# Kernel optimization log

Measured on AMD Instinct MI355X. Metric: run time of the kernel, lower is better.

The kernel has to match this reference:

```python
import jax, jax.numpy as jnp
import numpy as np

H = 128   # hidden_size
NL = 3    # num_layers
R = 32    # water_rows (Water2sea_slice_num)
O = 48    # water_cols (Original_slice_len)
B = 64    # batch_size
F = 32    # input_size
L = R + O - 1  # Water2sea_slice_len (wavefront length)


def setup_inputs():
    key = jax.random.key(0)
    k1, k2, k3, k4 = jax.random.split(key, 4)
    stdv = 1.0 / np.sqrt(H)
    inp = jax.random.normal(k1, (B, R, O, F), dtype=jnp.float32)
    W_first = jax.random.uniform(k2, (6 * H, F + 2 * H), minval=-stdv, maxval=stdv, dtype=jnp.float32)
    W_other = jax.random.uniform(k3, (NL - 1, 6 * H, 4 * H), minval=-stdv, maxval=stdv, dtype=jnp.float32)
    Bias = jax.random.uniform(k4, (NL, 6 * H), minval=-stdv, maxval=stdv, dtype=jnp.float32)
    return {"input": inp, "W_first": W_first, "W_other": W_other, "Bias": Bias,
            "batch_size": B, "input_size": F, "flag": 0}


def _forward(inp, W_first, W_other, Bias, batch_size, input_size, flag):
    # permute: flag==0 -> [rows, batch, cols, feat]
    x = jnp.transpose(inp, (2, 0, 1, 3)) if flag == 1 else jnp.transpose(inp, (1, 0, 2, 3))
    Rn, bs, On, Fn = x.shape
    Ln = Rn + On - 1
    # wavefront-shifted input: row r occupies slices [r, r+On) (input_transfer)
    padded = jnp.pad(x, ((0, 0), (0, 0), (0, Rn - 1), (0, 0)))                 # [R,B,L,F]
    shifted = jax.vmap(lambda t, r: jnp.roll(t, r, axis=1))(padded, jnp.arange(Rn))
    a0 = shifted.reshape(Rn * bs, Ln, Fn)
    # bias applied to row-group g at slice s iff (s < Rn) and (g <= s)  [faithful to linear()]
    s_idx = jnp.arange(Ln)[:, None]
    g_idx = jnp.arange(Rn)[None, :]
    bias_mask = ((g_idx <= s_idx) & (s_idx < Rn)).astype(jnp.float32)          # [L,R]
    bias_mask = jnp.repeat(bias_mask, bs, axis=1)[..., None]                   # [L,RB,1]

    def run_layer(a, W, bvec):
        # a: [RB, L, feat]; W: [6H, feat+2H]; bvec: [6H]
        def step(carry, xs):
            h_row, h_col = carry
            a_s, m_s = xs
            z = jnp.concatenate([h_row, h_col, a_s], axis=-1)
            gate = z @ W.T + m_s * bvec                                        # [RB,6H]
            sig = jax.nn.sigmoid(gate[:, :4 * H])
            tnh = jnp.tanh(gate[:, 4 * H:])
            ur, orow, uc, ocol = jnp.split(sig, 4, axis=-1)
            ir, ic = jnp.split(tnh, 2, axis=-1)
            h_row_n = jnp.tanh((1.0 - ur) * h_row + ur * ir) * orow
            h_col_n = jnp.tanh((1.0 - uc) * h_col + uc * ic) * ocol
            out = jnp.concatenate([h_row_n, h_col_n], axis=-1)
            h_col_roll = jnp.roll(h_col_n, bs, axis=0)  # transfer col hidden to next row
            return (h_row_n, h_col_roll), (out, h_row_n, h_col_n)
        h0 = jnp.zeros((Rn * bs, H), a.dtype)
        _, (outs, hrows, hcols) = jax.lax.scan(step, (h0, h0), (jnp.swapaxes(a, 0, 1), bias_mask))
        return outs, hrows, hcols  # each [L, RB, *]

    row_saves, col_saves = [], []
    a = a0
    for layer in range(NL):
        W = W_first if layer == 0 else W_other[layer - 1]
        outs, hrows, hcols = run_layer(a, W, Bias[layer])
        hrows = hrows.reshape(Ln, Rn, bs, H)
        hcols = hcols.reshape(Ln, Rn, bs, H)
        # row r finishes at slice On-1+r; col hidden of last row-group saved for slices >= Rn-1
        row_saves.append(hrows[On - 1 + jnp.arange(Rn), jnp.arange(Rn)])       # [R,B,H]
        col_saves.append(hcols[Rn - 1:, Rn - 1])                               # [O,B,H]
        a = jnp.swapaxes(outs, 0, 1)                                           # [RB,L,2H]; dropout p=0 -> identity
    output_all_slice = a
    hidden_row_all = jnp.transpose(jnp.stack(row_saves), (2, 0, 1, 3))         # [B,NL,R,H]
    hidden_col_all = jnp.transpose(jnp.stack(col_saves), (2, 0, 1, 3))         # [B,NL,O,H]
    return output_all_slice, hidden_row_all, hidden_col_all


def reference(input, W_first, W_other, Bias, batch_size, input_size, flag):
    return _forward(input, W_first, W_other, Bias, batch_size, input_size, flag)
```

## Files before the change

kernel.cpp:

```cpp
#include <hip/hip_runtime.h>
#include <stdint.h>

#define HH   128
#define NLAY 3
#define RR   32
#define OO   48
#define BBX  64
#define FFX  32
#define LLX  (RR + OO - 1)
#define RBr  (RR * BBX)
#define N6   (6 * HH)
#define TSTEPS (LLX + NLAY - 1)
#define NBLOCKS 192

typedef unsigned short u16;
typedef __attribute__((ext_vector_type(8))) short short8;
typedef __attribute__((ext_vector_type(4))) float f32x4;

#define OFF_ABUF0 ((size_t)0)
#define SZ_ABUF0  ((size_t)LLX * RBr * FFX * 2)
#define OFF_HZ    (OFF_ABUF0 + SZ_ABUF0)
#define SZ_HZ     ((size_t)NLAY * 2 * RBr * 256 * 2)
#define OFF_BAR   (OFF_HZ + SZ_HZ)
#define SZ_BAR    ((size_t)4096)
#define SZ_STATE  (SZ_HZ + SZ_BAR)

__device__ __forceinline__ u16 f2b(float x) {
  uint32_t u = __float_as_uint(x);
  return (u16)((u + 0x7FFFu + ((u >> 16) & 1u)) >> 16);
}
__device__ __forceinline__ float rcp_(float x) { return __builtin_amdgcn_rcpf(x); }
__device__ __forceinline__ float sigmoidf_(float x) {
  return rcp_(1.0f + __expf(-x));
}
__device__ __forceinline__ float tanhf_(float x) {
  return 1.0f - 2.0f * rcp_(__expf(2.0f * x) + 1.0f);
}

__global__ __launch_bounds__(256) void k_prep_input(const float* __restrict__ inp,
                                                    u16* __restrict__ abuf0) {
  int idx = blockIdx.x * 256 + threadIdx.x;
  if (idx >= LLX * RBr * FFX) return;
  int f   = idx & (FFX - 1);
  int row = (idx >> 5) & (RBr - 1);
  int s   = idx / (RBr * FFX);
  int g = row >> 6, b = row & 63;
  int o = s - g;
  float v = (o >= 0 && o < OO) ? inp[((b * RR + g) * OO + o) * FFX + f] : 0.0f;
  abuf0[idx] = f2b(v);
}

__global__ __launch_bounds__(256) void k_zero(uint32_t* __restrict__ p, size_t nwords) {
  size_t i = (size_t)blockIdx.x * 256 + threadIdx.x;
  size_t stride = (size_t)gridDim.x * 256;
  for (; i < nwords; i += stride) p[i] = 0u;
}

__device__ __forceinline__ void step_barrier(uint32_t* barC, uint32_t target, bool light) {
  __syncthreads();
  if (threadIdx.x == 0) {
    if (!light) __threadfence();
    __hip_atomic_fetch_add(barC, 1u, __ATOMIC_RELAXED, __HIP_MEMORY_SCOPE_AGENT);
    while (__hip_atomic_load(barC, __ATOMIC_RELAXED, __HIP_MEMORY_SCOPE_AGENT) < target)
      __builtin_amdgcn_s_sleep(1);
    if (!light) __threadfence();
  }
  __syncthreads();
  if (light) asm volatile("buffer_inv" ::: "memory");
}

template <int KK>
__device__ __forceinline__ void stage_w(const float* __restrict__ Wsrc, int jblk,
                                        u16* __restrict__ Wl) {
  constexpr int NFRAG = (KK / 32) * 6;
  for (int e = threadIdx.x; e < NFRAG * 64; e += 1024) {
    int kcm = e >> 6, ln = e & 63;
    int kc = kcm / 6, m = kcm - kc * 6;
    int fr2 = ln & 15, hi2 = ln >> 4;
    int srow = m * 128 + jblk * 16 + fr2;
    const float* src = Wsrc + (size_t)srow * KK + kc * 32 + hi2 * 8;
    short8 v;
#pragma unroll
    for (int x = 0; x < 8; ++x) v[x] = (short)f2b(src[x]);
    *(short8*)&Wl[(size_t)e * 8] = v;
  }
}

template <int KK>
__device__ __forceinline__ void persist_body(char* __restrict__ ws,
                                             const float* __restrict__ Bias_l,
                                             float* __restrict__ out,
                                             int layer, int jblk, int bblk, bool light,
                                             u16* __restrict__ Wl,
                                             float* __restrict__ hcl,
                                             uint32_t* __restrict__ barC) {
  constexpr int NCH = KK / 32;
  const int tid = threadIdx.x;
  const int lane = tid & 63, w = tid >> 6;
  const int fr = lane & 15, hi = lane >> 4;

  const int g0   = w * 2 + (fr >> 3);
  const int bcol = bblk * 8 + (fr & 7);
  const int arow = g0 * 64 + bcol;
  const int arp  = ((g0 + 1) & 31) * 64 + bcol;
  const int j = jblk * 16 + fr;
  const u16* wfrag = &Wl[lane * 8];
  float bia[6];
#pragma unroll
  for (int m = 0; m < 6; ++m) bia[m] = Bias_l[m * 128 + j];

  u16*   hz_base  = (u16*)(ws + OFF_HZ) + (size_t)layer * 2 * RBr * 256;
  u16*   hzp_base = (u16*)(ws + OFF_HZ) + (size_t)(layer - 1) * 2 * RBr * 256;
  u16*   abuf0    = (u16*)(ws + OFF_ABUF0);
  float* hid_row  = out + (size_t)RBr * LLX * 256;
  float* hid_col  = hid_row + (size_t)BBX * NLAY * RR * HH;

  float hr_reg[4];
#pragma unroll
  for (int q = 0; q < 4; ++q) hr_reg[q] = 0.0f;

  for (int t = 0; t < TSTEPS; ++t) {
    const int s = t - layer;
    if (s >= 0 && s < LLX) {
      const int sW = s & 1, sR = sW ^ 1;
      const u16* hzR = hz_base + (size_t)sR * RBr * 256;
      u16*       hzW = hz_base + (size_t)sW * RBr * 256;
      const u16* hzP = hzp_base + (size_t)sW * RBr * 256;
      const u16* ab_s = abuf0 + (size_t)s * RBr * FFX;
      const float* hcR = hcl + sR * 4352;
      float*       hcW = hcl + sW * 4352;

      if (w * 2 <= s) {
        auto LDK = [&](int kc) -> short8 {
          if (kc < 8)
            return *(const short8*)&hzR[arow * 256 + kc * 32 + hi * 8];
          if constexpr (KK == 288) {
            return *(const short8*)&ab_s[arow * FFX + hi * 8];
          } else {
            if (kc < 12)
              return *(const short8*)&hzP[arow * 256 + (kc - 8) * 32 + hi * 8];
            return *(const short8*)&hzP[arp * 256 + 128 + (kc - 12) * 32 + hi * 8];
          }
        };

        f32x4 z4 = {0.f, 0.f, 0.f, 0.f};
        f32x4 acc[6];
#pragma unroll
        for (int m = 0; m < 6; ++m) acc[m] = z4;

        short8 ring[3];
        ring[0] = LDK(0);
        ring[1] = LDK(1);
        ring[2] = LDK(2);
        __builtin_amdgcn_s_setprio(1);
#pragma unroll
        for (int kc = 0; kc < NCH; ++kc) {
          short8 a = ring[kc % 3];
          if (kc + 3 < NCH) ring[kc % 3] = LDK(kc + 3);
#pragma unroll
          for (int m = 0; m < 6; ++m) {
            short8 bv = *(const short8*)&wfrag[(size_t)(kc * 6 + m) * 512];
            acc[m] = __builtin_amdgcn_mfma_f32_16x16x32_bf16(a, bv, acc[m], 0, 0, 0);
          }
        }
        __builtin_amdgcn_s_setprio(0);

        const int g = w * 2 + (hi >> 1);
        const int gp = (g + 1) & (RR - 1);
        const float msk = (g <= s && s < RR) ? 1.0f : 0.0f;
        float mb[6];
#pragma unroll
        for (int m = 0; m < 6; ++m) mb[m] = msk * bia[m];
#pragma unroll
        for (int q = 0; q < 4; ++q) {
          const int lb = (hi & 1) * 4 + q;
          const int b  = bblk * 8 + lb;
          const int row = g * 64 + b;
          const int lrow = g * 8 + lb;
          const int rp = gp * 64 + b;
          const int lrp = gp * 8 + lb;
          float ur  = sigmoidf_(acc[0][q] + mb[0]);
          float orw = sigmoidf_(acc[1][q] + mb[1]);
          float uc  = sigmoidf_(acc[2][q] + mb[2]);
          float oc  = sigmoidf_(acc[3][q] + mb[3]);
          float ir  = tanhf_(acc[4][q] + mb[4]);
          float ic  = tanhf_(acc[5][q] + mb[5]);
          float hr_o = hr_reg[q];
          float hc_o = hcR[lrow * 17 + fr];
          float hr_n = tanhf_((1.0f - ur) * hr_o + ur * ir) * orw;
          float hc_n = tanhf_((1.0f - uc) * hc_o + uc * ic) * oc;
          hr_reg[q] = hr_n;
          hcW[lrp * 17 + fr] = hc_n;
          hzW[row * 256 + j] = f2b(hr_n);
          hzW[rp * 256 + HH + j] = f2b(hc_n);
          if (layer == 2) {
            out[((size_t)row * LLX + s) * 256 + j] = hr_n;
            out[((size_t)row * LLX + s) * 256 + HH + j] = hc_n;
          }
          if (s - g == OO - 1)
            hid_row[((size_t)(b * NLAY + layer) * RR + g) * HH + j] = hr_n;
          if (g == RR - 1 && s >= RR - 1)
            hid_col[((size_t)(b * NLAY + layer) * OO + (s - (RR - 1))) * HH + j] = hc_n;
        }
      } else {
        const int g = w * 2 + (hi >> 1);
        const int gp = (g + 1) & (RR - 1);
#pragma unroll
        for (int q = 0; q < 4; ++q) {
          const int lb = (hi & 1) * 4 + q;
          const int b  = bblk * 8 + lb;
          const int row = g * 64 + b;
          const int rp = gp * 64 + b;
          const int lrp = gp * 8 + lb;
          hcW[lrp * 17 + fr] = 0.0f;
          hzW[row * 256 + j] = 0;
          hzW[rp * 256 + HH + j] = 0;
          if (layer == 2) {
            out[((size_t)row * LLX + s) * 256 + j] = 0.0f;
            out[((size_t)row * LLX + s) * 256 + HH + j] = 0.0f;
          }
        }
      }
    }
    step_barrier(barC, 24u * (uint32_t)(t + 1), light);
  }
}

__global__ __launch_bounds__(1024, 4) void k_persist(char* __restrict__ ws,
                                                     const float* __restrict__ Wf,
                                                     const float* __restrict__ Wo,
                                                     const float* __restrict__ Bias,
                                                     float* __restrict__ out) {
  __shared__ u16 Wl[49152];
  __shared__ float hcl[8704];
  __shared__ uint32_t sh_light;
  const int bx = blockIdx.x;
  const int layer = bx >> 6, jblk = (bx >> 3) & 7, bblk = bx & 7;
  const int tid = threadIdx.x;

  if (layer == 0) stage_w<288>(Wf, jblk, Wl);
  else            stage_w<512>(Wo + (size_t)(layer - 1) * N6 * 512, jblk, Wl);
  for (int e = tid; e < 8704; e += 1024) hcl[e] = 0.0f;

  uint32_t xcc;
  asm volatile("s_getreg_b32 %0, hwreg(20, 0, 4)" : "=s"(xcc));
  uint32_t* barG  = (uint32_t*)(ws + OFF_BAR);
  uint32_t* barC  = (uint32_t*)(ws + OFF_BAR + 128 + (size_t)bblk * 128);
  uint32_t* table = (uint32_t*)(ws + OFF_BAR + 2048);
  __syncthreads();
  if (tid == 0) {
    __hip_atomic_store(&table[bx], xcc, __ATOMIC_RELAXED, __HIP_MEMORY_SCOPE_AGENT);
    __hip_atomic_fetch_add(barG, 1u, __ATOMIC_RELEASE, __HIP_MEMORY_SCOPE_AGENT);
    while (__hip_atomic_load(barG, __ATOMIC_ACQUIRE, __HIP_MEMORY_SCOPE_AGENT) < NBLOCKS)
      __builtin_amdgcn_s_sleep(1);
    uint32_t lt = 1u;
    for (int q2 = 0; q2 < 24; ++q2) {
      uint32_t v = __hip_atomic_load(&table[q2 * 8 + bblk], __ATOMIC_RELAXED,
                                     __HIP_MEMORY_SCOPE_AGENT);
      lt &= (v == xcc) ? 1u : 0u;
    }
    sh_light = lt;
  }
  __syncthreads();
  const bool light = (sh_light != 0u);

  const float* bias_l = Bias + layer * N6;
  if (layer == 0)
    persist_body<288>(ws, bias_l, out, 0, jblk, bblk, light, Wl, hcl, barC);
  else
    persist_body<512>(ws, bias_l, out, layer, jblk, bblk, light, Wl, hcl, barC);
}

extern "C" void kernel_launch(void* const* d_in, const int* in_sizes, int n_in,
                              void* d_out, int out_size, void* d_ws, size_t ws_size,
                              hipStream_t stream) {
  const float* inp  = (const float*)d_in[0];
  const float* Wf   = (const float*)d_in[1];
  const float* Wo   = (const float*)d_in[2];
  const float* Bias = (const float*)d_in[3];
  float* out = (float*)d_out;
  char* ws = (char*)d_ws;
  (void)in_sizes; (void)n_in; (void)out_size; (void)ws_size;

  k_prep_input<<<(LLX * RBr * FFX) / 256, 256, 0, stream>>>(inp, (u16*)(ws + OFF_ABUF0));
  k_zero<<<2048, 256, 0, stream>>>((uint32_t*)(ws + OFF_HZ), SZ_STATE / 4);
  k_persist<<<NBLOCKS, 1024, 0, stream>>>(ws, Wf, Wo, Bias, out);
}
```

Measured before the change: 770.8 us.

## Replace atomic-counter barrier with flag/epoch barrier and overlap output stores

Replaces the shared fetch-add step barrier with per-block arrival flags on separate cache lines, polled by a leader block that then publishes an epoch word all others spin on. The fp32 output and hidden-state stores move after the arrival signal, so they overlap the barrier wait instead of delaying it. The A-operand load ring is deepened from 3 to 6 stages. In exchange the barrier has an extra hop through the leader, and the deeper ring uses more registers.

```diff
diff --git a/kernel.cpp b/kernel.cpp
--- a/kernel.cpp
+++ b/kernel.cpp
@@ -22,7 +22,7 @@
 #define OFF_HZ    (OFF_ABUF0 + SZ_ABUF0)
 #define SZ_HZ     ((size_t)NLAY * 2 * RBr * 256 * 2)
 #define OFF_BAR   (OFF_HZ + SZ_HZ)
-#define SZ_BAR    ((size_t)4096)
+#define SZ_BAR    ((size_t)32768)
 #define SZ_STATE  (SZ_HZ + SZ_BAR)
 
 __device__ __forceinline__ u16 f2b(float x) {
@@ -56,19 +56,6 @@
   for (; i < nwords; i += stride) p[i] = 0u;
 }
 
-__device__ __forceinline__ void step_barrier(uint32_t* barC, uint32_t target, bool light) {
-  __syncthreads();
-  if (threadIdx.x == 0) {
-    if (!light) __threadfence();
-    __hip_atomic_fetch_add(barC, 1u, __ATOMIC_RELAXED, __HIP_MEMORY_SCOPE_AGENT);
-    while (__hip_atomic_load(barC, __ATOMIC_RELAXED, __HIP_MEMORY_SCOPE_AGENT) < target)
-      __builtin_amdgcn_s_sleep(1);
-    if (!light) __threadfence();
-  }
-  __syncthreads();
-  if (light) asm volatile("buffer_inv" ::: "memory");
-}
-
 template <int KK>
 __device__ __forceinline__ void stage_w(const float* __restrict__ Wsrc, int jblk,
                                         u16* __restrict__ Wl) {
@@ -93,11 +80,15 @@
                                              int layer, int jblk, int bblk, bool light,
                                              u16* __restrict__ Wl,
                                              float* __restrict__ hcl,
-                                             uint32_t* __restrict__ barC) {
+                                             uint32_t* __restrict__ arrC,
+                                             uint32_t* __restrict__ epoC,
+                                             bool leader) {
   constexpr int NCH = KK / 32;
+  constexpr int RD  = 6;
   const int tid = threadIdx.x;
   const int lane = tid & 63, w = tid >> 6;
   const int fr = lane & 15, hi = lane >> 4;
+  const int myslot = layer * 8 + jblk;
 
   const int g0   = w * 2 + (fr >> 3);
   const int bcol = bblk * 8 + (fr & 7);
@@ -121,6 +112,11 @@
 
   for (int t = 0; t < TSTEPS; ++t) {
     const int s = t - layer;
+    const uint32_t target = (uint32_t)(t + 1);
+    float sv_r[4], sv_c[4];
+#pragma unroll
+    for (int q = 0; q < 4; ++q) { sv_r[q] = 0.0f; sv_c[q] = 0.0f; }
+
     if (s >= 0 && s < LLX) {
       const int sW = s & 1, sR = sW ^ 1;
       const u16* hzR = hz_base + (size_t)sR * RBr * 256;
@@ -148,15 +144,14 @@
 #pragma unroll
         for (int m = 0; m < 6; ++m) acc[m] = z4;
 
-        short8 ring[3];
-        ring[0] = LDK(0);
-        ring[1] = LDK(1);
-        ring[2] = LDK(2);
+        short8 ring[RD];
+#pragma unroll
+        for (int i = 0; i < RD && i < NCH; ++i) ring[i] = LDK(i);
         __builtin_amdgcn_s_setprio(1);
 #pragma unroll
         for (int kc = 0; kc < NCH; ++kc) {
-          short8 a = ring[kc % 3];
-          if (kc + 3 < NCH) ring[kc % 3] = LDK(kc + 3);
+          short8 a = ring[kc % RD];
+          if (kc + RD < NCH) ring[kc % RD] = LDK(kc + RD);
 #pragma unroll
           for (int m = 0; m < 6; ++m) {
             short8 bv = *(const short8*)&wfrag[(size_t)(kc * 6 + m) * 512];
@@ -190,17 +185,11 @@
           float hr_n = tanhf_((1.0f - ur) * hr_o + ur * ir) * orw;
           float hc_n = tanhf_((1.0f - uc) * hc_o + uc * ic) * oc;
           hr_reg[q] = hr_n;
+          sv_r[q] = hr_n;
+          sv_c[q] = hc_n;
           hcW[lrp * 17 + fr] = hc_n;
           hzW[row * 256 + j] = f2b(hr_n);
           hzW[rp * 256 + HH + j] = f2b(hc_n);
-          if (layer == 2) {
-            out[((size_t)row * LLX + s) * 256 + j] = hr_n;
-            out[((size_t)row * LLX + s) * 256 + HH + j] = hc_n;
-          }
-          if (s - g == OO - 1)
-            hid_row[((size_t)(b * NLAY + layer) * RR + g) * HH + j] = hr_n;
-          if (g == RR - 1 && s >= RR - 1)
-            hid_col[((size_t)(b * NLAY + layer) * OO + (s - (RR - 1))) * HH + j] = hc_n;
         }
       } else {
         const int g = w * 2 + (hi >> 1);
@@ -215,14 +204,52 @@
           hcW[lrp * 17 + fr] = 0.0f;
           hzW[row * 256 + j] = 0;
           hzW[rp * 256 + HH + j] = 0;
-          if (layer == 2) {
-            out[((size_t)row * LLX + s) * 256 + j] = 0.0f;
-            out[((size_t)row * LLX + s) * 256 + HH + j] = 0.0f;
-          }
         }
       }
     }
-    step_barrier(barC, 24u * (uint32_t)(t + 1), light);
+
+    __syncthreads();
+    if (tid == 0) {
+      if (!light) __threadfence();
+      __hip_atomic_store(&arrC[myslot * 16], target, __ATOMIC_RELAXED,
+                         __HIP_MEMORY_SCOPE_AGENT);
+    }
+
+    if (s >= 0 && s < LLX) {
+      const int g = w * 2 + (hi >> 1);
+#pragma unroll
+      for (int q = 0; q < 4; ++q) {
+        const int lb = (hi & 1) * 4 + q;
+        const int b  = bblk * 8 + lb;
+        const int row = g * 64 + b;
+        if (layer == 2) {
+          out[((size_t)row * LLX + s) * 256 + j] = sv_r[q];
+          out[((size_t)row * LLX + s) * 256 + HH + j] = sv_c[q];
+        }
+        if (s - g == OO - 1)
+          hid_row[((size_t)(b * NLAY + layer) * RR + g) * HH + j] = sv_r[q];
+        if (g == RR - 1 && s >= RR - 1)
+          hid_col[((size_t)(b * NLAY + layer) * OO + (s - (RR - 1))) * HH + j] = sv_c[q];
+      }
+    }
+
+    if (leader) {
+      if (tid < 24) {
+        while (__hip_atomic_load(&arrC[tid * 16], __ATOMIC_RELAXED,
+                                 __HIP_MEMORY_SCOPE_AGENT) < target)
+          __builtin_amdgcn_s_sleep(1);
+      }
+      __syncthreads();
+      if (tid == 0)
+        __hip_atomic_store(epoC, target, __ATOMIC_RELAXED, __HIP_MEMORY_SCOPE_AGENT);
+    }
+    if (tid == 0) {
+      while (__hip_atomic_load(epoC, __ATOMIC_RELAXED, __HIP_MEMORY_SCOPE_AGENT) < target)
+        __builtin_amdgcn_s_sleep(1);
+      if (!light) __threadfence();
+    }
+    __syncthreads();
+    if (light) asm volatile("buffer_inv" ::: "memory");
   }
 }
 
@@ -245,8 +272,10 @@
   uint32_t xcc;
   asm volatile("s_getreg_b32 %0, hwreg(20, 0, 4)" : "=s"(xcc));
   uint32_t* barG  = (uint32_t*)(ws + OFF_BAR);
-  uint32_t* barC  = (uint32_t*)(ws + OFF_BAR + 128 + (size_t)bblk * 128);
-  uint32_t* table = (uint32_t*)(ws + OFF_BAR + 2048);
+  uint32_t* table = (uint32_t*)(ws + OFF_BAR + 256);
+  uint32_t* arrC  = (uint32_t*)(ws + OFF_BAR + 4096 + (size_t)bblk * 2048);
+  uint32_t* epoC  = (uint32_t*)(ws + OFF_BAR + 24576 + (size_t)bblk * 256);
+  const bool leader = (layer == 0 && jblk == 0);
   __syncthreads();
   if (tid == 0) {
     __hip_atomic_store(&table[bx], xcc, __ATOMIC_RELAXED, __HIP_MEMORY_SCOPE_AGENT);
@@ -266,9 +295,11 @@
 
   const float* bias_l = Bias + layer * N6;
   if (layer == 0)
-    persist_body<288>(ws, bias_l, out, 0, jblk, bblk, light, Wl, hcl, barC);
+    persist_body<288>(ws, bias_l, out, 0, jblk, bblk, light, Wl, hcl,
+                      arrC, epoC, leader);
   else
-    persist_body<512>(ws, bias_l, out, layer, jblk, bblk, light, Wl, hcl, barC);
+    persist_body<512>(ws, bias_l, out, layer, jblk, bblk, light, Wl, hcl,
+                      arrC, epoC, leader);
 }
 
 extern "C" void kernel_launch(void* const* d_in, const int* in_sizes, int n_in,
```

Result: faster. 730.2 us (-5.3%).
